# Kernel optimization log

Measured on AMD Instinct MI355X. Metric: run time of the kernel, lower is better.

The kernel has to match this reference:

```python
import jax, jax.numpy as jnp
from jax import lax
import numpy as np

ANCHOR_LENGTHS = (2.0, 4.0, 6.0, 9.0, 13.0, 18.0)  # A = 6


def make_anchors_1d(Lf, anchor_lengths):
    # anchors on the feature axis: [Lf*A, 2] (start, end)
    al = jnp.asarray(anchor_lengths, dtype=jnp.float32)          # [A]
    centers = jnp.arange(Lf, dtype=jnp.float32) + 0.5            # [Lf]
    start = centers[:, None] - 0.5 * al[None, :]                 # [Lf, A]
    end = centers[:, None] + 0.5 * al[None, :]                   # [Lf, A]
    return jnp.stack([start, end], axis=-1).reshape(Lf * al.shape[0], 2)


def setup_inputs() -> dict:
    key = jax.random.key(0)
    ks = jax.random.split(key, 4)
    B, C, Lf, A = 4, 512, 8192, len(ANCHOR_LENGTHS)
    feat = jax.random.normal(ks[0], (B, C, Lf), dtype=jnp.float32)
    conv_w = jax.random.normal(ks[1], (C, C, 3), dtype=jnp.float32) * 0.02   # OIW
    conv_b = jnp.zeros((C,), dtype=jnp.float32)
    obj_w = jax.random.normal(ks[2], (A, C, 1), dtype=jnp.float32) * 0.02
    obj_b = jnp.zeros((A,), dtype=jnp.float32)
    reg_w = jax.random.normal(ks[3], (A * 2, C, 1), dtype=jnp.float32) * 0.02
    reg_b = jnp.zeros((A * 2,), dtype=jnp.float32)
    return {"feat": feat, "conv_w": conv_w, "conv_b": conv_b,
            "obj_w": obj_w, "obj_b": obj_b, "reg_w": reg_w, "reg_b": reg_b}


def reference(feat, conv_w, conv_b, obj_w, obj_b, reg_w, reg_b):
    B, C, Lf = feat.shape
    A = obj_w.shape[0]
    # 3x1 conv, padding=1 -> SAME; layout N C W / O I W
    h = lax.conv_general_dilated(feat, conv_w, window_strides=(1,),
                                 padding="SAME",
                                 dimension_numbers=("NCH", "OIH", "NCH"))
    h = jax.nn.relu(h + conv_b[None, :, None])                   # [B, C, Lf]
    # 1x1 conv heads expressed as channel contractions
    obj = jnp.einsum("bcl,ac->bal", h, obj_w[:, :, 0]) + obj_b[None, :, None]   # [B, A, Lf]
    reg = jnp.einsum("bcl,ac->bal", h, reg_w[:, :, 0]) + reg_b[None, :, None]   # [B, 2A, Lf]
    obj = obj.transpose(0, 2, 1).reshape(B, Lf * A)                              # [B, N]
    reg = reg.transpose(0, 2, 1).reshape(B, Lf, A, 2).reshape(B, Lf * A, 2)      # [B, N, 2]
    anchors = make_anchors_1d(Lf, ANCHOR_LENGTHS)                                # [N, 2]
    return obj, reg, anchors
```

## Files before the change

kernel.cpp:

```cpp
#include <hip/hip_runtime.h>
#include <stdint.h>

typedef __attribute__((ext_vector_type(8))) short short8;
typedef __attribute__((ext_vector_type(4))) float f32x4;
typedef __attribute__((ext_vector_type(4))) float float4v;
typedef __attribute__((ext_vector_type(2))) unsigned short u16x2;
typedef __attribute__((ext_vector_type(4))) unsigned short u16x4;
typedef __attribute__((ext_vector_type(8))) unsigned short u16x8;

#define AS1 __attribute__((address_space(1)))
#define AS3 __attribute__((address_space(3)))


__device__ __forceinline__ unsigned short f2bf(float f) {
    union { float f; unsigned int u; } v; v.f = f;
    unsigned int r = v.u + 0x7fffu + ((v.u >> 16) & 1u);
    return (unsigned short)(r >> 16);
}

__constant__ float c_AL[6] = {2.f, 4.f, 6.f, 9.f, 13.f, 18.f};

__global__ __launch_bounds__(256) void prep_transpose_kernel(
    const float* __restrict__ feat, const float* __restrict__ conv_w,
    const float* __restrict__ obj_w, const float* __restrict__ reg_w,
    unsigned short* __restrict__ wAf, unsigned short* __restrict__ hwp,
    unsigned short* __restrict__ featT, float* __restrict__ out) {
    __shared__ unsigned short tile[64][66];
    unsigned int bx = blockIdx.x;
    int tid = threadIdx.x;
    if (bx < 4096u) {
        int l0 = (bx & 127) * 64, c0 = ((bx >> 7) & 7) * 64, b = bx >> 10;
        const float* fb = feat + ((size_t)b * 512 + c0) * 8192 + l0;
        #pragma unroll
        for (int it = 0; it < 4; ++it) {
            int slot = it * 256 + tid;
            int c = slot >> 4, l4 = (slot & 15) << 2;
            float4v v = *(const float4v*)(fb + (size_t)c * 8192 + l4);
            u16x2 p0, p1;
            p0.x = f2bf(v.x); p0.y = f2bf(v.y);
            p1.x = f2bf(v.z); p1.y = f2bf(v.w);
            *(u16x2*)(&tile[c][l4])     = p0;
            *(u16x2*)(&tile[c][l4 + 2]) = p1;
        }
        __syncthreads();
        unsigned short* ftb = featT + ((size_t)b * 8208 + 1 + l0) * 512 + c0;
        int c8 = tid & 7, lp = tid >> 3;
        unsigned int w[8];
        #pragma unroll
        for (int j = 0; j < 8; ++j)
            w[j] = *(const unsigned int*)(&tile[c8 * 8 + j][lp * 2]);
        u16x8 lo, hi;
        #pragma unroll
        for (int d = 0; d < 4; ++d) {
            unsigned int a = w[2 * d], bb = w[2 * d + 1];
            ((unsigned int*)&lo)[d] = (a & 0xffffu) | (bb << 16);
            ((unsigned int*)&hi)[d] = (a >> 16) | (bb & 0xffff0000u);
        }
        *(u16x8*)(ftb + (size_t)(lp * 2) * 512 + c8 * 8)     = lo;
        *(u16x8*)(ftb + (size_t)(lp * 2 + 1) * 512 + c8 * 8) = hi;
        return;
    }
    unsigned int idx = (bx - 4096u) * 256 + tid;
    if (idx < 196608u) {
        unsigned int base = idx * 4u;
        unsigned int chunkid = base >> 9;
        unsigned int within = base & 511u;
        unsigned int lane = within >> 3, j0 = within & 7u;
        unsigned int kc = chunkid & 15u;
        unsigned int ct = chunkid >> 4;
        unsigned int t = ct % 3u, cb = ct / 3u;
        unsigned int cout = cb * 16u + (lane & 15u);
        unsigned int cin0 = kc * 32u + (lane >> 4) * 8u + j0;
        const float* src = conv_w + (size_t)(cout * 512u + cin0) * 3u + t;
        u16x4 pk;
        pk.x = f2bf(src[0]);
        pk.y = f2bf(src[3]);
        pk.z = f2bf(src[6]);
        pk.w = f2bf(src[9]);
        *(u16x4*)(wAf + base) = pk;
    } else if (idx < 212992u) {
        unsigned int i2 = idx - 196608u;
        unsigned int j = i2 >> 9, c = i2 & 511u;
        float v = 0.f;
        if (j < 6u) v = obj_w[j * 512u + c];
        else if (j < 18u) v = reg_w[(j - 6u) * 512u + c];
        hwp[i2] = f2bf(v);
    } else if (idx < 262144u) {
        unsigned int n = idx - 212992u;
        unsigned int l = n / 6u, a = n - l * 6u;
        float ctr = (float)l + 0.5f, half = 0.5f * c_AL[a];
        float* anchors = out + 589824;
        anchors[2 * n]     = ctr - half;
        anchors[2 * n + 1] = ctr + half;
    } else if (idx < 266240u) {
        unsigned int i4 = idx - 262144u;
        unsigned int b = i4 >> 10, rem = i4 & 1023u;
        unsigned int row = (rem >> 9) ? 8193u : 0u;
        unsigned int c = rem & 511u;
        featT[((size_t)b * 8208 + row) * 512 + c] = 0;
    }
}

__global__ __launch_bounds__(256, 4) void conv_gemm_kernel(
    const unsigned short* __restrict__ wAf,
    const unsigned short* __restrict__ featT,
    const float* __restrict__ conv_b,
    const unsigned short* __restrict__ hwp,
    float* __restrict__ part) {
    __shared__ unsigned short smem[17408];

    const int tid = threadIdx.x;
    const int wave = tid >> 6, lane = tid & 63;
    const int lq = lane >> 4, lr = lane & 15;
    const int l0 = blockIdx.x * 128;
    const int m0 = blockIdx.y * 128;
    const int b = blockIdx.z;
    const int wm = wave >> 1, wn = wave & 1;
    const unsigned short* ftb = featT + (size_t)b * 8208 * 512;
    const unsigned short* wAb =
        wAf + ((size_t)((m0 >> 4) + wm * 4) * 3) * 16 * 512 + lane * 8;

    f32x4 acc[4][4];
    #pragma unroll
    for (int i = 0; i < 4; ++i)
        #pragma unroll
        for (int j = 0; j < 4; ++j)
            acc[i][j] = (f32x4){0.f, 0.f, 0.f, 0.f};

    for (int kc = 0; kc < 16; ++kc) {
        __syncthreads();
        for (int ci = wave; ci < 9; ci += 4) {
            const unsigned short* g =
                ftb + (size_t)(l0 + ci * 16 + lr) * 512 + kc * 32 + lq * 8;
            __builtin_amdgcn_global_load_lds((const AS1 void*)g,
                                             (AS3 void*)(smem + ci * 512), 16, 0, 0);
        }
        __syncthreads();
        #pragma unroll
        for (int t = 0; t < 3; ++t) {
            short8 af[4], bf[4];
            #pragma unroll
            for (int fm = 0; fm < 4; ++fm)
                af[fm] = *(const short8*)(wAb + ((size_t)((fm * 3 + t) * 16 + kc) << 9));
            #pragma unroll
            for (int fn = 0; fn < 4; ++fn) {
                int R = wn * 64 + fn * 16 + lr + t;
                bf[fn] = *(const short8*)(smem + ((R >> 4) << 9) +
                                          ((((lq << 4) | (R & 15))) << 3));
            }
            #pragma unroll
            for (int fm = 0; fm < 4; ++fm)
                #pragma unroll
                for (int fn = 0; fn < 4; ++fn)
                    acc[fm][fn] = __builtin_amdgcn_mfma_f32_16x16x32_bf16(
                        af[fm], bf[fn], acc[fm][fn], 0, 0, 0);
        }
    }
    __syncthreads();
    #pragma unroll
    for (int fm = 0; fm < 4; ++fm) {
        int mb = wm * 64 + fm * 16 + lq * 4;
        float cb0 = conv_b[m0 + mb];
        float cb1 = conv_b[m0 + mb + 1];
        float cb2 = conv_b[m0 + mb + 2];
        float cb3 = conv_b[m0 + mb + 3];
        #pragma unroll
        for (int fn = 0; fn < 4; ++fn) {
            int n = wn * 64 + fn * 16 + lr;
            f32x4 v = acc[fm][fn];
            u16x4 pk;
            pk.x = f2bf(fmaxf(v.x + cb0, 0.f));
            pk.y = f2bf(fmaxf(v.y + cb1, 0.f));
            pk.z = f2bf(fmaxf(v.z + cb2, 0.f));
            pk.w = f2bf(fmaxf(v.w + cb3, 0.f));
            *(u16x4*)(smem + n * 136 + mb) = pk;
        }
    }
    __syncthreads();
    f32x4 hacc[2][2];
    #pragma unroll
    for (int i = 0; i < 2; ++i) {
        hacc[i][0] = (f32x4){0.f, 0.f, 0.f, 0.f};
        hacc[i][1] = (f32x4){0.f, 0.f, 0.f, 0.f};
    }
    const int lbase = wave * 32;
    for (int kk = 0; kk < 4; ++kk) {
        short8 ha[2], hb2[2];
        #pragma unroll
        for (int fm2 = 0; fm2 < 2; ++fm2)
            ha[fm2] = *(const short8*)(smem + (lbase + fm2 * 16 + lr) * 136 + kk * 32 + lq * 8);
        #pragma unroll
        for (int fn = 0; fn < 2; ++fn)
            hb2[fn] = *(const short8*)(hwp + (size_t)(fn * 16 + lr) * 512 + m0 + kk * 32 + lq * 8);
        #pragma unroll
        for (int fm2 = 0; fm2 < 2; ++fm2)
            #pragma unroll
            for (int fn = 0; fn < 2; ++fn)
                hacc[fm2][fn] = __builtin_amdgcn_mfma_f32_16x16x32_bf16(
                    ha[fm2], hb2[fn], hacc[fm2][fn], 0, 0, 0);
    }
    float* pb = part + ((size_t)(blockIdx.y * 4 + b) * 8192) * 18;
    #pragma unroll
    for (int fn = 0; fn < 2; ++fn) {
        int j = fn * 16 + lr;
        if (j >= 18) continue;
        #pragma unroll
        for (int fm2 = 0; fm2 < 2; ++fm2)
            #pragma unroll
            for (int r = 0; r < 4; ++r) {
                int l = l0 + lbase + fm2 * 16 + lq * 4 + r;
                pb[(size_t)l * 18 + j] = hacc[fm2][fn][r];
            }
    }
}

__global__ __launch_bounds__(256) void reduce_kernel(
    const float* __restrict__ part, const float* __restrict__ obj_b,
    const float* __restrict__ reg_b, float* __restrict__ out) {
    unsigned int idx = blockIdx.x * 256 + threadIdx.x;
    unsigned int l = idx & 8191u, b = idx >> 13;
    float s[18];
    #pragma unroll
    for (int j = 0; j < 18; ++j) s[j] = 0.f;
    #pragma unroll
    for (int mb = 0; mb < 4; ++mb) {
        const float* p = part + ((size_t)(mb * 4 + b) * 8192 + l) * 18;
        #pragma unroll
        for (int j = 0; j < 18; ++j) s[j] += p[j];
    }
    float* ob = out + (size_t)b * 49152 + (size_t)l * 6;
    #pragma unroll
    for (int j = 0; j < 6; ++j) ob[j] = s[j] + obj_b[j];
    float* rg = out + 196608 + (size_t)b * 98304 + (size_t)l * 12;
    #pragma unroll
    for (int j = 0; j < 12; ++j) rg[j] = s[6 + j] + reg_b[j];
}

extern "C" void kernel_launch(void* const* d_in, const int* in_sizes, int n_in,
                              void* d_out, int out_size, void* d_ws, size_t ws_size,
                              hipStream_t stream) {
    const float* feat   = (const float*)d_in[0];
    const float* conv_w = (const float*)d_in[1];
    const float* conv_b = (const float*)d_in[2];
    const float* obj_w  = (const float*)d_in[3];
    const float* obj_b  = (const float*)d_in[4];
    const float* reg_w  = (const float*)d_in[5];
    const float* reg_b  = (const float*)d_in[6];
    float* out = (float*)d_out;
    char* ws = (char*)d_ws;
    unsigned short* wAf   = (unsigned short*)(ws);
    unsigned short* hwp   = (unsigned short*)(ws + 1572864);
    unsigned short* featT = (unsigned short*)(ws + 1605632);
    float* part           = (float*)(ws + 35225600);

    prep_transpose_kernel<<<dim3(5136), dim3(256), 0, stream>>>(
        feat, conv_w, obj_w, reg_w, wAf, hwp, featT, out);
    conv_gemm_kernel<<<dim3(64, 4, 4), dim3(256), 0, stream>>>(wAf, featT, conv_b, hwp, part);
    reduce_kernel<<<dim3(128), dim3(256), 0, stream>>>(part, obj_b, reg_b, out);
}
```

Measured before the change: 165.2 us.

## Double-buffer conv GEMM B tiles and split head epilogue into halves

Replaces the single shared B buffer with two ping-pong buffers. The next k-chunk's global-to-LDS load is issued before the current chunk's MFMAs, which removes one barrier per iteration and overlaps the load latency. Weight fragments for all three taps are hoisted to the start of each step. The epilogue now writes the ReLU tile into a smaller buffer in two 64-channel halves so the total LDS footprint stays similar. The cost is more registers for the hoisted A fragments and extra barriers in the epilogue.

```diff
diff --git a/kernel.cpp b/kernel.cpp
--- a/kernel.cpp
+++ b/kernel.cpp
@@ -107,7 +107,9 @@
     const float* __restrict__ conv_b,
     const unsigned short* __restrict__ hwp,
     float* __restrict__ part) {
-    __shared__ unsigned short smem[17408];
+    __shared__ unsigned short Bb0[4608];
+    __shared__ unsigned short Bb1[4608];
+    __shared__ unsigned short htile2[9216];
 
     const int tid = threadIdx.x;
     const int wave = tid >> 6, lane = tid & 63;
@@ -127,25 +129,33 @@
         for (int j = 0; j < 4; ++j)
             acc[i][j] = (f32x4){0.f, 0.f, 0.f, 0.f};
 
-    for (int kc = 0; kc < 16; ++kc) {
-        __syncthreads();
+    auto stageB = [&](int kc, unsigned short* dst) {
         for (int ci = wave; ci < 9; ci += 4) {
             const unsigned short* g =
                 ftb + (size_t)(l0 + ci * 16 + lr) * 512 + kc * 32 + lq * 8;
             __builtin_amdgcn_global_load_lds((const AS1 void*)g,
-                                             (AS3 void*)(smem + ci * 512), 16, 0, 0);
-        }
-        __syncthreads();
+                                             (AS3 void*)(dst + ci * 512), 16, 0, 0);
+        }
+    };
+
+    auto kstep = [&](int kc, unsigned short* curB, unsigned short* nxtB) {
+        short8 af[3][4];
+        #pragma unroll
+        for (int t = 0; t < 3; ++t)
+            #pragma unroll
+            for (int fm = 0; fm < 4; ++fm)
+                af[t][fm] = *(const short8*)(
+                    wAb + ((size_t)((fm * 3 + t) * 16 + kc) << 9));
+        __builtin_amdgcn_sched_barrier(0);
+        if (kc < 15) stageB(kc + 1, nxtB);
+        __builtin_amdgcn_sched_barrier(0);
         #pragma unroll
         for (int t = 0; t < 3; ++t) {
-            short8 af[4], bf[4];
-            #pragma unroll
-            for (int fm = 0; fm < 4; ++fm)
-                af[fm] = *(const short8*)(wAb + ((size_t)((fm * 3 + t) * 16 + kc) << 9));
+            short8 bf[4];
             #pragma unroll
             for (int fn = 0; fn < 4; ++fn) {
                 int R = wn * 64 + fn * 16 + lr + t;
-                bf[fn] = *(const short8*)(smem + ((R >> 4) << 9) +
+                bf[fn] = *(const short8*)(curB + ((R >> 4) << 9) +
                                           ((((lq << 4) | (R & 15))) << 3));
             }
             #pragma unroll
@@ -153,30 +163,19 @@
                 #pragma unroll
                 for (int fn = 0; fn < 4; ++fn)
                     acc[fm][fn] = __builtin_amdgcn_mfma_f32_16x16x32_bf16(
-                        af[fm], bf[fn], acc[fm][fn], 0, 0, 0);
-        }
-    }
+                        af[t][fm], bf[fn], acc[fm][fn], 0, 0, 0);
+        }
+        __syncthreads();
+    };
+
+    stageB(0, Bb0);
     __syncthreads();
-    #pragma unroll
-    for (int fm = 0; fm < 4; ++fm) {
-        int mb = wm * 64 + fm * 16 + lq * 4;
-        float cb0 = conv_b[m0 + mb];
-        float cb1 = conv_b[m0 + mb + 1];
-        float cb2 = conv_b[m0 + mb + 2];
-        float cb3 = conv_b[m0 + mb + 3];
-        #pragma unroll
-        for (int fn = 0; fn < 4; ++fn) {
-            int n = wn * 64 + fn * 16 + lr;
-            f32x4 v = acc[fm][fn];
-            u16x4 pk;
-            pk.x = f2bf(fmaxf(v.x + cb0, 0.f));
-            pk.y = f2bf(fmaxf(v.y + cb1, 0.f));
-            pk.z = f2bf(fmaxf(v.z + cb2, 0.f));
-            pk.w = f2bf(fmaxf(v.w + cb3, 0.f));
-            *(u16x4*)(smem + n * 136 + mb) = pk;
-        }
-    }
-    __syncthreads();
+    #pragma unroll 1
+    for (int k2 = 0; k2 < 8; ++k2) {
+        kstep(2 * k2,     Bb0, Bb1);
+        kstep(2 * k2 + 1, Bb1, Bb0);
+    }
+
     f32x4 hacc[2][2];
     #pragma unroll
     for (int i = 0; i < 2; ++i) {
@@ -184,20 +183,50 @@
         hacc[i][1] = (f32x4){0.f, 0.f, 0.f, 0.f};
     }
     const int lbase = wave * 32;
-    for (int kk = 0; kk < 4; ++kk) {
-        short8 ha[2], hb2[2];
-        #pragma unroll
-        for (int fm2 = 0; fm2 < 2; ++fm2)
-            ha[fm2] = *(const short8*)(smem + (lbase + fm2 * 16 + lr) * 136 + kk * 32 + lq * 8);
-        #pragma unroll
-        for (int fn = 0; fn < 2; ++fn)
-            hb2[fn] = *(const short8*)(hwp + (size_t)(fn * 16 + lr) * 512 + m0 + kk * 32 + lq * 8);
-        #pragma unroll
-        for (int fm2 = 0; fm2 < 2; ++fm2)
+    #pragma unroll
+    for (int mh = 0; mh < 2; ++mh) {
+        if (wm == mh) {
+            #pragma unroll
+            for (int fm = 0; fm < 4; ++fm) {
+                int mb = fm * 16 + lq * 4;
+                int cg = m0 + mh * 64 + mb;
+                float cb0 = conv_b[cg];
+                float cb1 = conv_b[cg + 1];
+                float cb2 = conv_b[cg + 2];
+                float cb3 = conv_b[cg + 3];
+                #pragma unroll
+                for (int fn = 0; fn < 4; ++fn) {
+                    int n = wn * 64 + fn * 16 + lr;
+                    f32x4 v = acc[fm][fn];
+                    u16x4 pk;
+                    pk.x = f2bf(fmaxf(v.x + cb0, 0.f));
+                    pk.y = f2bf(fmaxf(v.y + cb1, 0.f));
+                    pk.z = f2bf(fmaxf(v.z + cb2, 0.f));
+                    pk.w = f2bf(fmaxf(v.w + cb3, 0.f));
+                    *(u16x4*)(htile2 + n * 72 + mb) = pk;
+                }
+            }
+        }
+        __syncthreads();
+        #pragma unroll
+        for (int kk = 0; kk < 2; ++kk) {
+            short8 ha[2], hb2[2];
+            #pragma unroll
+            for (int fm2 = 0; fm2 < 2; ++fm2)
+                ha[fm2] = *(const short8*)(
+                    htile2 + (lbase + fm2 * 16 + lr) * 72 + kk * 32 + lq * 8);
             #pragma unroll
             for (int fn = 0; fn < 2; ++fn)
-                hacc[fm2][fn] = __builtin_amdgcn_mfma_f32_16x16x32_bf16(
-                    ha[fm2], hb2[fn], hacc[fm2][fn], 0, 0, 0);
+                hb2[fn] = *(const short8*)(
+                    hwp + (size_t)(fn * 16 + lr) * 512 + m0 + mh * 64 + kk * 32 + lq * 8);
+            #pragma unroll
+            for (int fm2 = 0; fm2 < 2; ++fm2)
+                #pragma unroll
+                for (int fn = 0; fn < 2; ++fn)
+                    hacc[fm2][fn] = __builtin_amdgcn_mfma_f32_16x16x32_bf16(
+                        ha[fm2], hb2[fn], hacc[fm2][fn], 0, 0, 0);
+        }
+        __syncthreads();
     }
     float* pb = part + ((size_t)(blockIdx.y * 4 + b) * 8192) * 18;
     #pragma unroll
```

Result: slower. 270.5 us (+63.7%).
